# Kernel tuning notes

Measured on AMD Instinct MI355X. Metric: run time of the kernel, lower is better.

Reference implementation:

```python
import jax, jax.numpy as jnp
import numpy as np

DIM = 512
NUM_HEADS = 8
HEAD_DIM = DIM // NUM_HEADS
GAMMA = 1.0


def setup_inputs() -> dict:
    key = jax.random.key(0)
    ks = jax.random.split(key, 10)
    B, S = 2, 2048
    x_real = jax.random.normal(ks[0], (B, S, DIM), dtype=jnp.float32)
    x_imag = jax.random.normal(ks[1], (B, S, DIM), dtype=jnp.float32)
    def xavier(k, fan_in, fan_out):
        lim = float(np.sqrt(6.0 / (fan_in + fan_out)))
        return jax.random.uniform(k, (fan_in, fan_out), jnp.float32, -lim, lim)
    # torch Linear(in,out): weight [out,in]; we store transposed [in,out]
    Wq = xavier(ks[2], 2 * DIM, DIM); bq = jnp.zeros((DIM,), jnp.float32)
    Wk = xavier(ks[3], 2 * DIM, DIM); bk = jnp.zeros((DIM,), jnp.float32)
    Wv = xavier(ks[4], 2 * DIM, DIM); bv = jnp.zeros((DIM,), jnp.float32)
    Wo = xavier(ks[5], DIM, 2 * DIM); bo = jnp.zeros((2 * DIM,), jnp.float32)
    return {"x_real": x_real, "x_imag": x_imag, "Wq": Wq, "bq": bq,
            "Wk": Wk, "bk": bk, "Wv": Wv, "bv": bv, "Wo": Wo, "bo": bo}


def reference(x_real, x_imag, Wq, bq, Wk, bk, Wv, bv, Wo, bo):
    B, S, _ = x_real.shape
    real_embed = jnp.concatenate([x_real, x_imag], axis=-1)  # [B,S,2*dim]
    def proj(W, b):
        y = real_embed @ W + b                               # [B,S,dim]
        return y.reshape(B, S, NUM_HEADS, HEAD_DIM).transpose(0, 2, 1, 3)  # [B,H,S,d]
    Q = proj(Wq, bq)
    K = proj(Wk, bk)
    V = proj(Wv, bv)
    # softmax over head_dim is broadcast-invariant, so the Bhattacharyya
    # coefficient sum_d sqrt(p_i[d]*q_j[d]) factorizes into a matmul.
    sp = jnp.sqrt(jax.nn.softmax(Q, axis=-1))  # [B,H,S,d]
    sq = jnp.sqrt(jax.nn.softmax(K, axis=-1))  # [B,H,S,d]
    bc = jnp.einsum('bhid,bhjd->bhij', sp, sq)  # Bhattacharyya coeff [B,H,S,S]
    bc = jnp.clip(bc, -1.0, 1.0)
    dist = jnp.arccos(bc)
    attn = jax.nn.softmax(-GAMMA * dist * dist, axis=-1)  # [B,H,S,S]
    attended = jnp.einsum('bhij,bhjd->bhid', attn, V)
    attended = attended.transpose(0, 2, 1, 3).reshape(B, S, DIM)
    out = attended @ Wo + bo  # [B,S,2*dim] = concat(real_out, imag_out)
    return out
```

## Files before the change

kernel.cpp:

```cpp
#include <hip/hip_runtime.h>
#include <math.h>


typedef __attribute__((ext_vector_type(8))) short short8;
typedef __attribute__((ext_vector_type(4))) short bf16x4;
typedef __attribute__((ext_vector_type(4))) float f32x4;
typedef __attribute__((ext_vector_type(2))) float f32x2;
typedef __attribute__((ext_vector_type(4))) unsigned int u32x4;

#define MFMA(a, b, c) __builtin_amdgcn_mfma_f32_16x16x32_bf16((a), (b), (c), 0, 0, 0)

static __device__ __forceinline__ short f2bf(float f) {
    unsigned u = __float_as_uint(f);
    u += 0x7fffu + ((u >> 16) & 1u);
    return (short)(u >> 16);
}

static __device__ __forceinline__ void gld_lds16(const short* g, short* l) {
    __builtin_amdgcn_global_load_lds(
        (const __attribute__((address_space(1))) unsigned int*)g,
        (__attribute__((address_space(3))) unsigned int*)l, 16, 0, 0);
}

__global__ __launch_bounds__(256) void convert_x(
    const float* __restrict__ xr, const float* __restrict__ xi,
    short* __restrict__ xb)
{
    int idx = blockIdx.x * 256 + threadIdx.x;
    int e = idx << 2;
    int m = e >> 10, k = e & 1023;
    const float* src = (k < 512) ? xr : xi;
    float4 t = *(const float4*)(src + (size_t)m * 512 + (k & 511));
    unsigned lo = (unsigned short)f2bf(t.x) | ((unsigned)(unsigned short)f2bf(t.y) << 16);
    unsigned hi = (unsigned short)f2bf(t.z) | ((unsigned)(unsigned short)f2bf(t.w) << 16);
    uint2 o; o.x = lo; o.y = hi;
    *(uint2*)(xb + e) = o;
}

__global__ __launch_bounds__(256) void transpose_w(
    const float* __restrict__ Wq, const float* __restrict__ Wk,
    const float* __restrict__ Wv, const float* __restrict__ Wo,
    short* __restrict__ wqt, short* __restrict__ wkt,
    short* __restrict__ wvt, short* __restrict__ wot)
{
    __shared__ float t[32][33];
    const int z = blockIdx.z;
    const float* src = (z == 0) ? Wq : (z == 1) ? Wk : (z == 2) ? Wv : Wo;
    short* dst = (z == 0) ? wqt : (z == 1) ? wkt : (z == 2) ? wvt : wot;
    const int K = (z < 3) ? 1024 : 512;
    const int N = (z < 3) ? 512 : 1024;
    const int n0 = blockIdx.x << 5, k0 = blockIdx.y << 5;
    if (n0 >= N || k0 >= K) return;
    const int tx = threadIdx.x & 31, ty = threadIdx.x >> 5;
    #pragma unroll
    for (int i = 0; i < 4; ++i)
        t[ty + 8 * i][tx] = src[(size_t)(k0 + ty + 8 * i) * N + n0 + tx];
    __syncthreads();
    #pragma unroll
    for (int i = 0; i < 4; ++i)
        dst[(size_t)(n0 + ty + 8 * i) * K + k0 + tx] = f2bf(t[tx][ty + 8 * i]);
}

__global__ __launch_bounds__(64) void qkv_mfma(
    const short* __restrict__ xb, const short* __restrict__ wcat,
    const float* __restrict__ bq, const float* __restrict__ bk,
    const float* __restrict__ bv,
    short* __restrict__ sp, short* __restrict__ sq, short* __restrict__ vt)
{
    __shared__ short As[3][64 * 32];
    __shared__ short Bs[3][64 * 32];
    const int jb = blockIdx.x;
    const int m0 = blockIdx.y << 6;
    const int lane = threadIdx.x;
    const int l = lane & 15, quad = lane >> 4;
    const int l7 = l & 7;

    const int srow = lane >> 2;
    const int sseg = (lane & 3) << 3;
    const short* gA = xb   + (size_t)(m0        + srow) * 1024 + sseg;
    const short* gB = wcat + (size_t)((jb << 6) + srow) * 1024 + sseg;

    auto STAGE = [&](int bb, int kk) {
        const int k0 = kk << 5;
        #pragma unroll
        for (int t = 0; t < 4; ++t) {
            gld_lds16(gA + k0 + t * 16 * 1024, &As[bb][t << 9]);
            gld_lds16(gB + k0 + t * 16 * 1024, &Bs[bb][t << 9]);
        }
    };

    STAGE(0, 0);
    STAGE(1, 1);
    asm volatile("s_waitcnt vmcnt(8)" ::: "memory");

    const f32x4 z4 = {0.f, 0.f, 0.f, 0.f};
    f32x4 acc[4][4];
    #pragma unroll
    for (int i = 0; i < 4; ++i)
        #pragma unroll
        for (int j = 0; j < 4; ++j) acc[i][j] = z4;

    int cb = 0, sb = 2;
    #pragma unroll 1
    for (int kt = 0; kt < 32; ++kt) {
        STAGE(sb, (kt + 2) & 31);
        const short* Al = &As[cb][0];
        const short* Bl = &Bs[cb][0];
        short8 af[4], bfr[4];
        #pragma unroll
        for (int i = 0; i < 4; ++i)
            af[i] = *(const short8*)(Al + (((i << 4) + l) << 5) + (quad << 3));
        #pragma unroll
        for (int j = 0; j < 4; ++j)
            bfr[j] = *(const short8*)(Bl + (((j << 4) + l) << 5) + (quad << 3));
        #pragma unroll
        for (int i = 0; i < 4; ++i)
            #pragma unroll
            for (int j = 0; j < 4; ++j)
                acc[i][j] = MFMA(af[i], bfr[j], acc[i][j]);
        asm volatile("s_waitcnt vmcnt(8)" ::: "memory");
        cb = (cb == 2) ? 0 : cb + 1;
        sb = (sb == 2) ? 0 : sb + 1;
    }

    const int op = jb >> 3;
    const int h  = jb & 7;

    if (op < 2) {
        short* dst = (op == 0) ? sp : sq;
        const float* bias = (op == 0) ? bq : bk;
        float bcol[4];
        #pragma unroll
        for (int nt = 0; nt < 4; ++nt) bcol[nt] = bias[(h << 6) + (nt << 4) + l];
        #pragma unroll
        for (int i = 0; i < 4; ++i) {
            #pragma unroll
            for (int reg = 0; reg < 4; ++reg) {
                const int r = m0 + (i << 4) + (quad << 2) + reg;
                const int b = r >> 11, s = r & 2047;
                float v[4];
                #pragma unroll
                for (int nt = 0; nt < 4; ++nt) v[nt] = acc[i][nt][reg] + bcol[nt];
                float mx = fmaxf(fmaxf(v[0], v[1]), fmaxf(v[2], v[3]));
                #pragma unroll
                for (int msk = 1; msk < 16; msk <<= 1) mx = fmaxf(mx, __shfl_xor(mx, msk));
                float e[4], ssum = 0.f;
                #pragma unroll
                for (int nt = 0; nt < 4; ++nt) { e[nt] = __expf(v[nt] - mx); ssum += e[nt]; }
                #pragma unroll
                for (int msk = 1; msk < 16; msk <<= 1) ssum += __shfl_xor(ssum, msk);
                float inv = 1.0f / ssum;
                short* o = dst + ((size_t)((b << 3) + h) * 2048 + s) * 64;
                if (op == 0) {
                    #pragma unroll
                    for (int nt = 0; nt < 4; ++nt)
                        o[(nt << 4) + l] = f2bf(sqrtf(e[nt] * inv));
                } else {
                    const int s7 = r & 7;
                    #pragma unroll
                    for (int nt = 0; nt < 4; ++nt)
                        o[((((nt << 1) + (l >> 3)) ^ s7) << 3) + l7] =
                            f2bf(sqrtf(e[nt] * inv));
                }
            }
        }
    } else {
        float bcol[4];
        #pragma unroll
        for (int nt = 0; nt < 4; ++nt) bcol[nt] = bv[(h << 6) + (nt << 4) + l];
        #pragma unroll
        for (int i = 0; i < 4; ++i) {
            const int sb2 = m0 + (i << 4) + (quad << 2);
            const int b = sb2 >> 11, s = sb2 & 2047;
            const int gg = (s >> 2) & 15;
            const int u = ((gg >> 3) << 2) + (gg & 3);
            const int colp = (s & ~63) + (((u ^ l7)) << 3) + (((gg >> 2) & 1) << 2);
            #pragma unroll
            for (int nt = 0; nt < 4; ++nt) {
                const int d = (nt << 4) + l;
                bf16x4 pk;
                #pragma unroll
                for (int reg = 0; reg < 4; ++reg)
                    pk[reg] = f2bf(acc[i][nt][reg] + bcol[nt]);
                *(bf16x4*)(vt + ((size_t)((b << 3) + h) * 64 + d) * 2048 + colp) = pk;
            }
        }
    }
}

__global__ __launch_bounds__(256, 4) void attn_mfma(
    const short* __restrict__ sp, const short* __restrict__ sq,
    const short* __restrict__ vt,
    float* __restrict__ pnum, float* __restrict__ pden)
{
    __shared__ __align__(16) short sqT[2][64 * 64];
    __shared__ __align__(16) short vtT[2][64 * 64];
    const int bh = blockIdx.y;
    const int m0 = blockIdx.x << 6;
    const int z  = blockIdx.z;
    const int tid = threadIdx.x;
    const int w = tid >> 6, lane = tid & 63;
    const int l = lane & 15, quad = lane >> 4;
    const int l7 = l & 7;

    const short* spB = sp + (size_t)bh * 2048 * 64;
    const short* sqB = sq + (size_t)bh * 2048 * 64;
    const short* vtB = vt + (size_t)bh * 64 * 2048;

    const short* apr = spB + (size_t)(m0 + w * 16 + l) * 64 + quad * 8;
    short8 nq0 = (*(const short8*)(apr)) ^ (short)0x8000;
    short8 nq1 = (*(const short8*)(apr + 32)) ^ (short)0x8000;

    const int lr = lane >> 3;
    const int lu = lane & 7;
    const int r0 = w << 1;

    auto STAGEATT = [&](int buf, int jrow) {
        #pragma unroll
        for (int k = 0; k < 2; ++k) {
            const int r = r0 + k;
            gld_lds16(sqB + (size_t)(jrow + (r << 3) + lr) * 64 + (lu << 3),
                      &sqT[buf][r << 9]);
            gld_lds16(vtB + (size_t)((r << 3) + lr) * 2048 + jrow + (lu << 3),
                      &vtT[buf][r << 9]);
        }
    };

    const int sRd = (quad ^ l7) << 3;

    STAGEATT(0, z << 10);
    __syncthreads();

    const f32x4 ones4 = {1.f, 1.f, 1.f, 1.f};
    const f32x4 z4 = {0.f, 0.f, 0.f, 0.f};
    f32x4 acc[4] = {z4, z4, z4, z4};
    f32x2 den2 = {0.f, 0.f};

    #pragma unroll 1
    for (int jtl = 0; jtl < 16; ++jtl) {
        const int cb = jtl & 1, nb = cb ^ 1;
        const int j0n = (z << 10) + (((jtl + 1) & 15) << 6);
        STAGEATT(nb, j0n);

        uint2 pk[4];
        const short* sqL = &sqT[cb][0];
        #pragma unroll
        for (int nt = 0; nt < 4; ++nt) {
            const short* ar = sqL + ((nt * 16 + l) << 6);
            short8 sa0 = *(const short8*)(ar + sRd);
            short8 sa1 = *(const short8*)(ar + (sRd ^ 32));
            f32x4 p = MFMA(sa0, nq0, ones4);
            p = MFMA(sa1, nq1, p);
            f32x2 u01 = {p[0], p[1]};
            f32x2 u23 = {p[2], p[3]};
            const f32x2 zz = {0.f, 0.f};
#if __has_builtin(__builtin_elementwise_max)
            u01 = __builtin_elementwise_max(u01, zz);
            u23 = __builtin_elementwise_max(u23, zz);
#else
            u01.x = fmaxf(u01.x, 0.f); u01.y = fmaxf(u01.y, 0.f);
            u23.x = fmaxf(u23.x, 0.f); u23.y = fmaxf(u23.y, 0.f);
#endif
            f32x2 t01 = {-0.00133017f, -0.00133017f};
            f32x2 t23 = t01;
            t01 = t01 * u01 - 0.00219618f;  t23 = t23 * u23 - 0.00219618f;
            t01 = t01 * u01 - 0.00555151f;  t23 = t23 * u23 - 0.00555151f;
            t01 = t01 * u01 - 0.01465597f;  t23 = t23 * u23 - 0.01465597f;
            t01 = t01 * u01 - 0.04121986f;  t23 = t23 * u23 - 0.04121986f;
            t01 = t01 * u01 - 0.12823956f;  t23 = t23 * u23 - 0.12823956f;
            t01 = t01 * u01 - 0.48089834f;  t23 = t23 * u23 - 0.48089834f;
            t01 = t01 * u01 - 2.88539008f;  t23 = t23 * u23 - 2.88539008f;
            f32x2 w01 = u01 * t01;
            f32x2 w23 = u23 * t23;
#if __has_builtin(__builtin_amdgcn_exp2f)
            float e0 = __builtin_amdgcn_exp2f(w01.x);
            float e1 = __builtin_amdgcn_exp2f(w01.y);
            float e2 = __builtin_amdgcn_exp2f(w23.x);
            float e3 = __builtin_amdgcn_exp2f(w23.y);
#else
            float e0 = exp2f(w01.x), e1 = exp2f(w01.y);
            float e2 = exp2f(w23.x), e3 = exp2f(w23.y);
#endif
            f32x2 es = {e0 + e2, e1 + e3};
            den2 += es;
            pk[nt].x = (__float_as_uint(e0) >> 16) | (__float_as_uint(e1) & 0xffff0000u);
            pk[nt].y = (__float_as_uint(e2) >> 16) | (__float_as_uint(e3) & 0xffff0000u);
        }

        u32x4 c0; c0.x = pk[0].x; c0.y = pk[0].y; c0.z = pk[1].x; c0.w = pk[1].y;
        u32x4 c1; c1.x = pk[2].x; c1.y = pk[2].y; c1.z = pk[3].x; c1.w = pk[3].y;
        short8 pa0 = __builtin_bit_cast(short8, c0);
        short8 pa1 = __builtin_bit_cast(short8, c1);
        const short* vL = &vtT[cb][0];
        #pragma unroll
        for (int t4 = 0; t4 < 4; ++t4) {
            const short* vr = vL + ((t4 * 16 + l) << 6);
            short8 vb0 = *(const short8*)(vr + sRd);
            short8 vb1 = *(const short8*)(vr + (sRd ^ 32));
            acc[t4] = MFMA(pa0, vb0, acc[t4]);
            acc[t4] = MFMA(pa1, vb1, acc[t4]);
        }

        __syncthreads();
    }

    float den = den2.x + den2.y;
    den += __shfl_xor(den, 16);
    den += __shfl_xor(den, 32);
    if (lane < 16)
        pden[(size_t)z * 32768 + bh * 2048 + m0 + w * 16 + l] = den;

    const int b = bh >> 3, hh = bh & 7;
    float* np = pnum + (size_t)z * 4096 * 512;
    #pragma unroll
    for (int t4 = 0; t4 < 4; ++t4)
        #pragma unroll
        for (int reg = 0; reg < 4; ++reg) {
            const int row = m0 + w * 16 + quad * 4 + reg;
            np[((size_t)(b * 2048 + row)) * 512 + hh * 64 + t4 * 16 + l] =
                acc[t4][reg];
        }
}

__global__ __launch_bounds__(256) void combine_attn(
    const float* __restrict__ pnum, const float* __restrict__ pden,
    short* __restrict__ attB)
{
    const int idx = (blockIdx.x * 256 + threadIdx.x) << 3;
    const int r = idx >> 9;
    const int c = idx & 511;
    const int hh = c >> 6;
    const int bh = ((r >> 11) << 3) + hh;
    const int srow = r & 2047;
    const float d = pden[bh * 2048 + srow] + pden[32768 + bh * 2048 + srow];
    const float inv = 1.0f / d;
    const float* n0 = pnum + (size_t)r * 512 + c;
    const float* n1 = n0 + (size_t)4096 * 512;
    float4 a0 = *(const float4*)(n0);
    float4 a1 = *(const float4*)(n0 + 4);
    float4 b0 = *(const float4*)(n1);
    float4 b1 = *(const float4*)(n1 + 4);
    short8 o;
    o[0] = f2bf((a0.x + b0.x) * inv);
    o[1] = f2bf((a0.y + b0.y) * inv);
    o[2] = f2bf((a0.z + b0.z) * inv);
    o[3] = f2bf((a0.w + b0.w) * inv);
    o[4] = f2bf((a1.x + b1.x) * inv);
    o[5] = f2bf((a1.y + b1.y) * inv);
    o[6] = f2bf((a1.z + b1.z) * inv);
    o[7] = f2bf((a1.w + b1.w) * inv);
    *(short8*)(attB + idx) = o;
}

__global__ __launch_bounds__(64) void out_mfma(
    const short* __restrict__ attB, const short* __restrict__ wot,
    const float* __restrict__ bo, float* __restrict__ out)
{
    __shared__ short As[3][64 * 32];
    __shared__ short Bs[3][64 * 32];
    const int n0 = blockIdx.x << 6;
    const int m0 = blockIdx.y << 6;
    const int lane = threadIdx.x;
    const int l = lane & 15, quad = lane >> 4;

    const int srow = lane >> 2;
    const int sseg = (lane & 3) << 3;
    const short* gA = attB + (size_t)(m0 + srow) * 512 + sseg;
    const short* gB = wot  + (size_t)(n0 + srow) * 512 + sseg;

    auto STAGE = [&](int bb, int kk) {
        const int k0 = kk << 5;
        #pragma unroll
        for (int t = 0; t < 4; ++t) {
            gld_lds16(gA + k0 + t * 16 * 512, &As[bb][t << 9]);
            gld_lds16(gB + k0 + t * 16 * 512, &Bs[bb][t << 9]);
        }
    };

    STAGE(0, 0);
    STAGE(1, 1);
    asm volatile("s_waitcnt vmcnt(8)" ::: "memory");

    const f32x4 z4 = {0.f, 0.f, 0.f, 0.f};
    f32x4 acc[4][4];
    #pragma unroll
    for (int i = 0; i < 4; ++i)
        #pragma unroll
        for (int j = 0; j < 4; ++j) acc[i][j] = z4;

    int cb = 0, sb = 2;
    #pragma unroll 1
    for (int kt = 0; kt < 16; ++kt) {
        STAGE(sb, (kt + 2) & 15);
        const short* Al = &As[cb][0];
        const short* Bl = &Bs[cb][0];
        short8 af[4], bfr[4];
        #pragma unroll
        for (int i = 0; i < 4; ++i)
            af[i] = *(const short8*)(Al + (((i << 4) + l) << 5) + (quad << 3));
        #pragma unroll
        for (int j = 0; j < 4; ++j)
            bfr[j] = *(const short8*)(Bl + (((j << 4) + l) << 5) + (quad << 3));
        #pragma unroll
        for (int i = 0; i < 4; ++i)
            #pragma unroll
            for (int j = 0; j < 4; ++j)
                acc[i][j] = MFMA(af[i], bfr[j], acc[i][j]);
        asm volatile("s_waitcnt vmcnt(8)" ::: "memory");
        cb = (cb == 2) ? 0 : cb + 1;
        sb = (sb == 2) ? 0 : sb + 1;
    }

    float bcol[4];
    #pragma unroll
    for (int nt = 0; nt < 4; ++nt) bcol[nt] = bo[n0 + (nt << 4) + l];
    #pragma unroll
    for (int i = 0; i < 4; ++i)
        #pragma unroll
        for (int reg = 0; reg < 4; ++reg) {
            const int m = m0 + (i << 4) + (quad << 2) + reg;
            float* o = out + (size_t)m * 1024 + n0 + l;
            #pragma unroll
            for (int nt = 0; nt < 4; ++nt)
                o[nt << 4] = acc[i][nt][reg] + bcol[nt];
        }
}

extern "C" void kernel_launch(void* const* d_in, const int* in_sizes, int n_in,
                              void* d_out, int out_size, void* d_ws, size_t ws_size,
                              hipStream_t stream) {
    const float* xr = (const float*)d_in[0];
    const float* xi = (const float*)d_in[1];
    const float* Wq = (const float*)d_in[2];
    const float* bq = (const float*)d_in[3];
    const float* Wk = (const float*)d_in[4];
    const float* bk = (const float*)d_in[5];
    const float* Wv = (const float*)d_in[6];
    const float* bv = (const float*)d_in[7];
    const float* Wo = (const float*)d_in[8];
    const float* bo = (const float*)d_in[9];
    float* out = (float*)d_out;

    short* base = (short*)d_ws;
    short* xb   = base;
    short* wqt  = xb  + 4194304;
    short* wkt  = wqt + 524288;
    short* wvt  = wkt + 524288;
    short* wot  = wvt + 524288;
    short* spW  = wot + 524288;
    short* sqW  = spW + 2097152;
    short* vtW  = sqW + 2097152;
    short* attB = vtW + 2097152;
    float* pnum = (float*)(attB + 2097152);
    float* pden = pnum + 8388608;

    hipLaunchKernelGGL(convert_x, dim3(4096), dim3(256), 0, stream, xr, xi, xb);
    hipLaunchKernelGGL(transpose_w, dim3(32, 32, 4), dim3(256), 0, stream,
                       Wq, Wk, Wv, Wo, wqt, wkt, wvt, wot);
    hipLaunchKernelGGL(qkv_mfma, dim3(24, 64), dim3(64), 0, stream,
                       xb, wqt, bq, bk, bv, spW, sqW, vtW);
    hipLaunchKernelGGL(attn_mfma, dim3(32, 16, 2), dim3(256), 0, stream,
                       spW, sqW, vtW, pnum, pden);
    hipLaunchKernelGGL(combine_attn, dim3(1024), dim3(256), 0, stream,
                       pnum, pden, attB);
    hipLaunchKernelGGL(out_mfma, dim3(16, 64), dim3(64), 0, stream,
                       attB, wot, bo, out);
}
```

Before: 187.5 us.

## Pre-tile swizzled bf16 operands, merge prep kernels, split attention keys four ways

Merges the x conversion and weight transpose into one prep kernel that writes operands in a tiled, XOR-swizzled layout. Each 64x32 GEMM stage then becomes one contiguous global-to-LDS copy, and LDS reads avoid bank conflicts. The attention kernel's key range is split into four chunks instead of two to double the grid. The combine kernel now sums four partials and writes attB in the tiled layout. This trades more partial-sum traffic for better occupancy and more efficient loads, at the cost of more complex indexing.

```diff
diff --git a/kernel.cpp b/kernel.cpp
--- a/kernel.cpp
+++ b/kernel.cpp
@@ -22,43 +22,63 @@
         (__attribute__((address_space(3))) unsigned int*)l, 16, 0, 0);
 }
 
-__global__ __launch_bounds__(256) void convert_x(
+__global__ __launch_bounds__(256) void prep_all(
     const float* __restrict__ xr, const float* __restrict__ xi,
-    short* __restrict__ xb)
-{
-    int idx = blockIdx.x * 256 + threadIdx.x;
-    int e = idx << 2;
-    int m = e >> 10, k = e & 1023;
-    const float* src = (k < 512) ? xr : xi;
-    float4 t = *(const float4*)(src + (size_t)m * 512 + (k & 511));
-    unsigned lo = (unsigned short)f2bf(t.x) | ((unsigned)(unsigned short)f2bf(t.y) << 16);
-    unsigned hi = (unsigned short)f2bf(t.z) | ((unsigned)(unsigned short)f2bf(t.w) << 16);
-    uint2 o; o.x = lo; o.y = hi;
-    *(uint2*)(xb + e) = o;
-}
-
-__global__ __launch_bounds__(256) void transpose_w(
+    short* __restrict__ xb,
     const float* __restrict__ Wq, const float* __restrict__ Wk,
     const float* __restrict__ Wv, const float* __restrict__ Wo,
-    short* __restrict__ wqt, short* __restrict__ wkt,
-    short* __restrict__ wvt, short* __restrict__ wot)
+    short* __restrict__ wqt, short* __restrict__ wot)
 {
-    __shared__ float t[32][33];
-    const int z = blockIdx.z;
-    const float* src = (z == 0) ? Wq : (z == 1) ? Wk : (z == 2) ? Wv : Wo;
-    short* dst = (z == 0) ? wqt : (z == 1) ? wkt : (z == 2) ? wvt : wot;
-    const int K = (z < 3) ? 1024 : 512;
-    const int N = (z < 3) ? 512 : 1024;
-    const int n0 = blockIdx.x << 5, k0 = blockIdx.y << 5;
-    if (n0 >= N || k0 >= K) return;
-    const int tx = threadIdx.x & 31, ty = threadIdx.x >> 5;
-    #pragma unroll
-    for (int i = 0; i < 4; ++i)
-        t[ty + 8 * i][tx] = src[(size_t)(k0 + ty + 8 * i) * N + n0 + tx];
-    __syncthreads();
-    #pragma unroll
-    for (int i = 0; i < 4; ++i)
-        dst[(size_t)(n0 + ty + 8 * i) * K + k0 + tx] = f2bf(t[tx][ty + 8 * i]);
+    const int bid = blockIdx.x;
+    if (bid < 2048) {
+        const unsigned wid = bid * 256 + threadIdx.x;
+        const int p  = wid & 7;
+        const int rp = (wid >> 3) & 31;
+        const int kt = (wid >> 8) & 31;
+        const int mb = wid >> 13;
+        const int up = p ^ (rp & 7);
+        const int m  = (mb << 6) | (rp << 1) | (up >> 2);
+        const int k  = (kt << 5) | ((up & 3) << 3);
+        const float* s = (k < 512) ? (xr + (size_t)m * 512 + k)
+                                   : (xi + (size_t)m * 512 + (k - 512));
+        float4 t0 = *(const float4*)(s);
+        float4 t1 = *(const float4*)(s + 4);
+        short8 o;
+        o[0] = f2bf(t0.x); o[1] = f2bf(t0.y); o[2] = f2bf(t0.z); o[3] = f2bf(t0.w);
+        o[4] = f2bf(t1.x); o[5] = f2bf(t1.y); o[6] = f2bf(t1.z); o[7] = f2bf(t1.w);
+        *(short8*)(xb + (size_t)wid * 8) = o;
+    } else {
+        __shared__ float tt[32][33];
+        const int t = bid - 2048;
+        const int z = t >> 9;
+        const int idx = t & 511;
+        const float* src = (z == 0) ? Wq : (z == 1) ? Wk : (z == 2) ? Wv : Wo;
+        const int N = (z < 3) ? 512 : 1024;
+        const int bx = (z < 3) ? (idx & 15) : (idx & 31);
+        const int by = (z < 3) ? (idx >> 4) : (idx >> 5);
+        const int n0 = bx << 5, k0 = by << 5;
+        const int tx = threadIdx.x & 31, ty = threadIdx.x >> 5;
+        #pragma unroll
+        for (int i = 0; i < 4; ++i)
+            tt[ty + 8 * i][tx] = src[(size_t)(k0 + ty + 8 * i) * N + n0 + tx];
+        __syncthreads();
+        const int k = k0 + tx;
+        const int kt = k >> 5, u = (k >> 3) & 3, off = k & 7;
+        #pragma unroll
+        for (int i = 0; i < 4; ++i) {
+            const int n = n0 + ty + 8 * i;
+            const int nb = n >> 6, rn = n & 63;
+            const int rp = rn >> 1;
+            const int up = ((rn & 1) << 2) | u;
+            const int p  = up ^ (rp & 7);
+            const float v = tt[tx][ty + 8 * i];
+            if (z < 3)
+                wqt[(size_t)z * 524288 +
+                    ((size_t)(nb * 32 + kt)) * 2048 + rp * 64 + p * 8 + off] = f2bf(v);
+            else
+                wot[((size_t)(nb * 16 + kt)) * 2048 + rp * 64 + p * 8 + off] = f2bf(v);
+        }
+    }
 }
 
 __global__ __launch_bounds__(64) void qkv_mfma(
@@ -70,22 +90,21 @@
     __shared__ short As[3][64 * 32];
     __shared__ short Bs[3][64 * 32];
     const int jb = blockIdx.x;
-    const int m0 = blockIdx.y << 6;
+    const int mb = blockIdx.y;
+    const int m0 = mb << 6;
     const int lane = threadIdx.x;
     const int l = lane & 15, quad = lane >> 4;
     const int l7 = l & 7;
 
-    const int srow = lane >> 2;
-    const int sseg = (lane & 3) << 3;
-    const short* gA = xb   + (size_t)(m0        + srow) * 1024 + sseg;
-    const short* gB = wcat + (size_t)((jb << 6) + srow) * 1024 + sseg;
+    const short* gA = xb   + (size_t)mb * 65536 + lane * 8;
+    const short* gB = wcat + (size_t)jb * 65536 + lane * 8;
 
     auto STAGE = [&](int bb, int kk) {
-        const int k0 = kk << 5;
+        const int k0 = kk << 11;
         #pragma unroll
         for (int t = 0; t < 4; ++t) {
-            gld_lds16(gA + k0 + t * 16 * 1024, &As[bb][t << 9]);
-            gld_lds16(gB + k0 + t * 16 * 1024, &Bs[bb][t << 9]);
+            gld_lds16(gA + k0 + t * 512, &As[bb][t << 9]);
+            gld_lds16(gB + k0 + t * 512, &Bs[bb][t << 9]);
         }
     };
 
@@ -99,6 +118,10 @@
     for (int i = 0; i < 4; ++i)
         #pragma unroll
         for (int j = 0; j < 4; ++j) acc[i][j] = z4;
+
+    const int rbase = (l >> 1) << 6;
+    const int pA = (((((l & 1) << 2) | quad) ^ ((l >> 1) & 7)) << 3);
+    const int rdo = rbase + pA;
 
     int cb = 0, sb = 2;
     #pragma unroll 1
@@ -109,10 +132,10 @@
         short8 af[4], bfr[4];
         #pragma unroll
         for (int i = 0; i < 4; ++i)
-            af[i] = *(const short8*)(Al + (((i << 4) + l) << 5) + (quad << 3));
+            af[i] = *(const short8*)(Al + (i << 9) + rdo);
         #pragma unroll
         for (int j = 0; j < 4; ++j)
-            bfr[j] = *(const short8*)(Bl + (((j << 4) + l) << 5) + (quad << 3));
+            bfr[j] = *(const short8*)(Bl + (j << 9) + rdo);
         #pragma unroll
         for (int i = 0; i < 4; ++i)
             #pragma unroll
@@ -228,7 +251,7 @@
 
     const int sRd = (quad ^ l7) << 3;
 
-    STAGEATT(0, z << 10);
+    STAGEATT(0, z << 9);
     __syncthreads();
 
     const f32x4 ones4 = {1.f, 1.f, 1.f, 1.f};
@@ -237,9 +260,9 @@
     f32x2 den2 = {0.f, 0.f};
 
     #pragma unroll 1
-    for (int jtl = 0; jtl < 16; ++jtl) {
+    for (int jtl = 0; jtl < 8; ++jtl) {
         const int cb = jtl & 1, nb = cb ^ 1;
-        const int j0n = (z << 10) + (((jtl + 1) & 15) << 6);
+        const int j0n = ((z << 3) + ((jtl + 1) & 7)) << 6;
         STAGEATT(nb, j0n);
 
         uint2 pk[4];
@@ -332,24 +355,31 @@
     const int hh = c >> 6;
     const int bh = ((r >> 11) << 3) + hh;
     const int srow = r & 2047;
-    const float d = pden[bh * 2048 + srow] + pden[32768 + bh * 2048 + srow];
+    float d = 0.f;
+    #pragma unroll
+    for (int zi = 0; zi < 4; ++zi)
+        d += pden[(size_t)zi * 32768 + bh * 2048 + srow];
     const float inv = 1.0f / d;
-    const float* n0 = pnum + (size_t)r * 512 + c;
-    const float* n1 = n0 + (size_t)4096 * 512;
-    float4 a0 = *(const float4*)(n0);
-    float4 a1 = *(const float4*)(n0 + 4);
-    float4 b0 = *(const float4*)(n1);
-    float4 b1 = *(const float4*)(n1 + 4);
+    float4 a0 = {0.f, 0.f, 0.f, 0.f}, a1 = {0.f, 0.f, 0.f, 0.f};
+    #pragma unroll
+    for (int zi = 0; zi < 4; ++zi) {
+        const float* n0 = pnum + (size_t)zi * 4096 * 512 + (size_t)r * 512 + c;
+        float4 b0 = *(const float4*)(n0);
+        float4 b1 = *(const float4*)(n0 + 4);
+        a0.x += b0.x; a0.y += b0.y; a0.z += b0.z; a0.w += b0.w;
+        a1.x += b1.x; a1.y += b1.y; a1.z += b1.z; a1.w += b1.w;
+    }
     short8 o;
-    o[0] = f2bf((a0.x + b0.x) * inv);
-    o[1] = f2bf((a0.y + b0.y) * inv);
-    o[2] = f2bf((a0.z + b0.z) * inv);
-    o[3] = f2bf((a0.w + b0.w) * inv);
-    o[4] = f2bf((a1.x + b1.x) * inv);
-    o[5] = f2bf((a1.y + b1.y) * inv);
-    o[6] = f2bf((a1.z + b1.z) * inv);
-    o[7] = f2bf((a1.w + b1.w) * inv);
-    *(short8*)(attB + idx) = o;
+    o[0] = f2bf(a0.x * inv); o[1] = f2bf(a0.y * inv);
+    o[2] = f2bf(a0.z * inv); o[3] = f2bf(a0.w * inv);
+    o[4] = f2bf(a1.x * inv); o[5] = f2bf(a1.y * inv);
+    o[6] = f2bf(a1.z * inv); o[7] = f2bf(a1.w * inv);
+    const int mb = r >> 6, rm = r & 63;
+    const int kt = c >> 5, u = (c >> 3) & 3;
+    const int rp = rm >> 1;
+    const int up = ((rm & 1) << 2) | u;
+    const int p  = up ^ (rp & 7);
+    *(short8*)(attB + ((size_t)(mb * 16 + kt)) * 2048 + rp * 64 + p * 8) = o;
 }
 
 __global__ __launch_bounds__(64) void out_mfma(
@@ -358,22 +388,22 @@
 {
     __shared__ short As[3][64 * 32];
     __shared__ short Bs[3][64 * 32];
-    const int n0 = blockIdx.x << 6;
-    const int m0 = blockIdx.y << 6;
+    const int nb = blockIdx.x;
+    const int mb = blockIdx.y;
+    const int n0 = nb << 6;
+    const int m0 = mb << 6;
     const int lane = threadIdx.x;
     const int l = lane & 15, quad = lane >> 4;
 
-    const int srow = lane >> 2;
-    const int sseg = (lane & 3) << 3;
-    const short* gA = attB + (size_t)(m0 + srow) * 512 + sseg;
-    const short* gB = wot  + (size_t)(n0 + srow) * 512 + sseg;
+    const short* gA = attB + (size_t)mb * 32768 + lane * 8;
+    const short* gB = wot  + (size_t)nb * 32768 + lane * 8;
 
     auto STAGE = [&](int bb, int kk) {
-        const int k0 = kk << 5;
+        const int k0 = kk << 11;
         #pragma unroll
         for (int t = 0; t < 4; ++t) {
-            gld_lds16(gA + k0 + t * 16 * 512, &As[bb][t << 9]);
-            gld_lds16(gB + k0 + t * 16 * 512, &Bs[bb][t << 9]);
+            gld_lds16(gA + k0 + t * 512, &As[bb][t << 9]);
+            gld_lds16(gB + k0 + t * 512, &Bs[bb][t << 9]);
         }
     };
 
@@ -387,6 +417,10 @@
     for (int i = 0; i < 4; ++i)
         #pragma unroll
         for (int j = 0; j < 4; ++j) acc[i][j] = z4;
+
+    const int rbase = (l >> 1) << 6;
+    const int pA = (((((l & 1) << 2) | quad) ^ ((l >> 1) & 7)) << 3);
+    const int rdo = rbase + pA;
 
     int cb = 0, sb = 2;
     #pragma unroll 1
@@ -397,10 +431,10 @@
         short8 af[4], bfr[4];
         #pragma unroll
         for (int i = 0; i < 4; ++i)
-            af[i] = *(const short8*)(Al + (((i << 4) + l) << 5) + (quad << 3));
+            af[i] = *(const short8*)(Al + (i << 9) + rdo);
         #pragma unroll
         for (int j = 0; j < 4; ++j)
-            bfr[j] = *(const short8*)(Bl + (((j << 4) + l) << 5) + (quad << 3));
+            bfr[j] = *(const short8*)(Bl + (j << 9) + rdo);
         #pragma unroll
         for (int i = 0; i < 4; ++i)
             #pragma unroll
@@ -444,22 +478,19 @@
     short* base = (short*)d_ws;
     short* xb   = base;
     short* wqt  = xb  + 4194304;
-    short* wkt  = wqt + 524288;
-    short* wvt  = wkt + 524288;
-    short* wot  = wvt + 524288;
+    short* wot  = wqt + 1572864;
     short* spW  = wot + 524288;
     short* sqW  = spW + 2097152;
     short* vtW  = sqW + 2097152;
     short* attB = vtW + 2097152;
     float* pnum = (float*)(attB + 2097152);
-    float* pden = pnum + 8388608;
-
-    hipLaunchKernelGGL(convert_x, dim3(4096), dim3(256), 0, stream, xr, xi, xb);
-    hipLaunchKernelGGL(transpose_w, dim3(32, 32, 4), dim3(256), 0, stream,
-                       Wq, Wk, Wv, Wo, wqt, wkt, wvt, wot);
+    float* pden = pnum + 4 * 2097152;
+
+    hipLaunchKernelGGL(prep_all, dim3(4096), dim3(256), 0, stream,
+                       xr, xi, xb, Wq, Wk, Wv, Wo, wqt, wot);
     hipLaunchKernelGGL(qkv_mfma, dim3(24, 64), dim3(64), 0, stream,
                        xb, wqt, bq, bk, bv, spW, sqW, vtW);
-    hipLaunchKernelGGL(attn_mfma, dim3(32, 16, 2), dim3(256), 0, stream,
+    hipLaunchKernelGGL(attn_mfma, dim3(32, 16, 4), dim3(256), 0, stream,
                        spW, sqW, vtW, pnum, pden);
     hipLaunchKernelGGL(combine_attn, dim3(1024), dim3(256), 0, stream,
                        pnum, pden, attB);
```

Measured after the change: 184.3 us. About the same (-1.7%).
